# Performance work log

Measured on AMD Instinct MI355X. Metric: run time of the kernel, lower is better.

The kernel has to match this reference:

```python
import jax, jax.numpy as jnp
import numpy as np

EPS = 1e-7  # keras backend epsilon

def setup_inputs() -> dict:
    key = jax.random.key(0)
    k1, k2, k3, k4, k5 = jax.random.split(key, 5)
    B, S, D, A = 64, 2048, 512, 256
    x = jax.random.normal(k1, (B, S, D), dtype=jnp.float32)
    mask = jax.random.randint(k2, (B, S), 0, 2) > 0
    # keras 'normal' initializer: RandomNormal(stddev=0.05)
    W = 0.05 * jax.random.normal(k3, (D, A), dtype=jnp.float32)
    b = 0.05 * jax.random.normal(k4, (A,), dtype=jnp.float32)
    u = 0.05 * jax.random.normal(k5, (A, 1), dtype=jnp.float32)
    return {"x": x, "mask": mask, "W": W, "b": b, "u": u}

def reference(x, mask, W, b, u):
    # x: [B,S,D], W: [D,A], b: [A], u: [A,1]
    uit = jnp.tanh(jnp.einsum('bsd,da->bsa', x, W) + b)   # [B,S,A]
    ait = jnp.einsum('bsa,a->bs', uit, u[:, 0])           # [B,S]
    ait = jnp.exp(ait)
    ait = ait * mask.astype(x.dtype)
    ait = ait / (jnp.sum(ait, axis=1, keepdims=True) + EPS)  # [B,S]
    return jnp.einsum('bsd,bs->bd', x, ait)               # [B,D]
```

## Files before the change

kernel.cpp:

```cpp
#include <hip/hip_runtime.h>
#include <stdint.h>

#define B_ 64
#define S_ 2048
#define D_ 512
#define A_ 256
#define TM 32
#define TPB 16
#define NBLK 256
#define EPS 1e-7f

typedef short bf16x8 __attribute__((ext_vector_type(8)));
typedef float f32x4  __attribute__((ext_vector_type(4)));

#define WS_WT   0
#define WS_PART 262144
#define WS_ZP   786432
#define WS_FLAG 787456

__device__ __forceinline__ uint32_t f32pair_to_bf16(float a, float b) {
  uint32_t ua = __float_as_uint(a), ub = __float_as_uint(b);
  ua = (ua + 0x7fffu + ((ua >> 16) & 1u)) >> 16;
  ub = (ub + 0x7fffu + ((ub >> 16) & 1u)) & 0xffff0000u;
  return ua | ub;
}

__global__ __launch_bounds__(256) void prep_kernel(
    const float* __restrict__ W, const void* __restrict__ mask,
    uint16_t* __restrict__ Wt, int* __restrict__ flag)
{
  int i = blockIdx.x * 256 + threadIdx.x;
  if (i < A_ * D_) {
    int a = i >> 9;
    int d = i & (D_ - 1);
    uint32_t u = __float_as_uint(W[d * A_ + a]);
    u = (u + 0x7fffu + ((u >> 16) & 1u)) >> 16;
    Wt[i] = (uint16_t)u;
  }
  if (blockIdx.x == 0 && threadIdx.x < 64) {
    const uint32_t* mw = (const uint32_t*)mask;
    int hit = 0;
    for (int k = 0; k < 16; ++k) {
      uint32_t v = mw[threadIdx.x + 64 * k];
      uint32_t b0 = v & 0xff, b1 = (v >> 8) & 0xff, b2 = (v >> 16) & 0xff, b3 = v >> 24;
      if (b0 <= 1u && b1 <= 1u && b2 <= 1u && b3 <= 1u && (b1 | b2 | b3)) hit = 1;
    }
    hit = __any(hit);
    if (threadIdx.x == 0) *flag = hit ? 1 : 0;
  }
}

__global__ __launch_bounds__(512, 2) void att_main(
    const float* __restrict__ x, const void* __restrict__ mask,
    const float* __restrict__ bias, const float* __restrict__ uvec,
    const uint16_t* __restrict__ Wt, float* __restrict__ part,
    float* __restrict__ Zpart, const int* __restrict__ flag)
{
  __shared__ uint16_t xs[2][TM * D_];
  __shared__ float sp[8][TM];
  __shared__ float ev[TM];

  const int tid = threadIdx.x;
  const int l  = tid & 63, w  = tid >> 6;
  const int lr = l & 15,   lg = l >> 4;
  const int bx = blockIdx.x;
  const int b  = bx >> 2;
  const int s0 = (bx & 3) * (TM * TPB);
  const float* xb = x + ((size_t)b * S_ + s0) * D_;
  const int mflag = *flag;

  bf16x8 bfr[32];
  {
    const uint16_t* wtb = Wt + (size_t)(w * 32 + lr) * D_;
    #pragma unroll
    for (int ks = 0; ks < 16; ++ks)
      #pragma unroll
      for (int nt = 0; nt < 2; ++nt)
        bfr[ks * 2 + nt] = *(const bf16x8*)(wtb + nt * 16 * D_ + ks * 32 + lg * 8);
  }
  float bn[2], un[2];
  #pragma unroll
  for (int nt = 0; nt < 2; ++nt) {
    int n = w * 32 + nt * 16 + lr;
    bn[nt] = bias[n];
    un[nt] = uvec[n];
  }

  float num_acc = 0.0f;
  float zacc    = 0.0f;

  float4 v[4][2];
  #pragma unroll
  for (int c = 0; c < 4; ++c) {
    int q = c * 512 + tid;
    const float* src = xb + (q >> 6) * D_ + (q & 63) * 8;
    v[c][0] = *(const float4*)src;
    v[c][1] = *(const float4*)(src + 4);
  }

  for (int t = 0; t < TPB; ++t) {
    uint16_t* buf = xs[t & 1];

    #pragma unroll
    for (int c = 0; c < 4; ++c) {
      int q = c * 512 + tid;
      int row = q >> 6, cb = q & 63;
      uint4 pk;
      pk.x = f32pair_to_bf16(v[c][0].x, v[c][0].y);
      pk.y = f32pair_to_bf16(v[c][0].z, v[c][0].w);
      pk.z = f32pair_to_bf16(v[c][1].x, v[c][1].y);
      pk.w = f32pair_to_bf16(v[c][1].z, v[c][1].w);
      *(uint4*)(&buf[row * D_ + (cb ^ (row & 7)) * 8]) = pk;
    }
    __syncthreads();

    if (t + 1 < TPB) {
      const float* xt = xb + (size_t)(t + 1) * TM * D_;
      #pragma unroll
      for (int c = 0; c < 4; ++c) {
        int q = c * 512 + tid;
        const float* src = xt + (q >> 6) * D_ + (q & 63) * 8;
        v[c][0] = *(const float4*)src;
        v[c][1] = *(const float4*)(src + 4);
      }
    }

    f32x4 acc[2][2];
    #pragma unroll
    for (int mt = 0; mt < 2; ++mt)
      #pragma unroll
      for (int nt = 0; nt < 2; ++nt)
        acc[mt][nt] = (f32x4){0.f, 0.f, 0.f, 0.f};

    #pragma unroll
    for (int ks = 0; ks < 16; ++ks) {
      bf16x8 af[2];
      #pragma unroll
      for (int mt = 0; mt < 2; ++mt)
        af[mt] = *(const bf16x8*)(&buf[(mt * 16 + lr) * D_ + (((ks * 4 + lg) ^ (lr & 7)) * 8)]);
      #pragma unroll
      for (int mt = 0; mt < 2; ++mt)
        #pragma unroll
        for (int nt = 0; nt < 2; ++nt)
          acc[mt][nt] = __builtin_amdgcn_mfma_f32_16x16x32_bf16(af[mt], bfr[ks * 2 + nt], acc[mt][nt], 0, 0, 0);
    }

    #pragma unroll
    for (int mt = 0; mt < 2; ++mt) {
      #pragma unroll
      for (int r = 0; r < 4; ++r) {
        float ssum = 0.0f;
        #pragma unroll
        for (int nt = 0; nt < 2; ++nt) {
          float vv = acc[mt][nt][r] + bn[nt];
          float av = fabsf(vv);
          float e2 = __expf(-2.0f * av);
          float th = 1.0f - 2.0f * e2 * __builtin_amdgcn_rcpf(1.0f + e2);
          ssum += copysignf(th, vv) * un[nt];
        }
        ssum += __shfl_xor(ssum, 1);
        ssum += __shfl_xor(ssum, 2);
        ssum += __shfl_xor(ssum, 4);
        ssum += __shfl_xor(ssum, 8);
        if (lr == 0) sp[w][mt * 16 + lg * 4 + r] = ssum;
      }
    }
    __syncthreads();

    if (tid < TM) {
      float score = 0.0f;
      #pragma unroll
      for (int ww = 0; ww < 8; ++ww) score += sp[ww][tid];
      int midx = b * S_ + s0 + t * TM + tid;
      int mv = mflag ? (((const unsigned char*)mask)[midx] != 0)
                     : (((const int*)mask)[midx] != 0);
      float e = mv ? __expf(score) : 0.0f;
      ev[tid] = e;
      float tot = e;
      #pragma unroll
      for (int o = 1; o < TM; o <<= 1) tot += __shfl_xor(tot, o);
      if (tid == 0) zacc += tot;
    }
    __syncthreads();

    {
      int c = tid >> 3, wo = (tid & 7) >> 1;
      #pragma unroll 8
      for (int s = 0; s < TM; ++s) {
        uint32_t vv = *(const uint32_t*)(&buf[s * D_ + (c ^ (s & 7)) * 8 + wo * 2]);
        float xv = (tid & 1) ? __uint_as_float(vv & 0xffff0000u)
                             : __uint_as_float(vv << 16);
        num_acc = fmaf(ev[s], xv, num_acc);
      }
    }
  }

  part[(size_t)bx * D_ + tid] = num_acc;
  if (tid == 0) Zpart[bx] = zacc;
}

__global__ __launch_bounds__(256) void scale_kernel(
    const float* __restrict__ part, const float* __restrict__ Zpart,
    float* __restrict__ out)
{
  int idx = blockIdx.x * 256 + threadIdx.x;
  int b = idx >> 9;
  int d = idx & (D_ - 1);
  float s = 0.0f, z = 0.0f;
  #pragma unroll
  for (int g = 0; g < 4; ++g) {
    s += part[(size_t)(b * 4 + g) * D_ + d];
    z += Zpart[b * 4 + g];
  }
  out[idx] = s / (z + EPS);
}

extern "C" void kernel_launch(void* const* d_in, const int* in_sizes, int n_in,
                              void* d_out, int out_size, void* d_ws, size_t ws_size,
                              hipStream_t stream)
{
  const float* x    = (const float*)d_in[0];
  const void*  mask = d_in[1];
  const float* W    = (const float*)d_in[2];
  const float* bias = (const float*)d_in[3];
  const float* u    = (const float*)d_in[4];
  float* out = (float*)d_out;

  char* ws = (char*)d_ws;
  uint16_t* Wt  = (uint16_t*)(ws + WS_WT);
  float* part   = (float*)(ws + WS_PART);
  float* Zpart  = (float*)(ws + WS_ZP);
  int*   flag   = (int*)(ws + WS_FLAG);

  prep_kernel<<<(A_ * D_ + 255) / 256, 256, 0, stream>>>(W, mask, Wt, flag);
  att_main<<<NBLK, 512, 0, stream>>>(x, mask, bias, u, Wt, part, Zpart, flag);
  scale_kernel<<<(B_ * D_ + 255) / 256, 256, 0, stream>>>(part, Zpart, out);
}
```

Before: 379.0 us.

## Stream x tiles via direct global-to-LDS loads and cut per-tile barriers

Replaces the register-staged prefetch of x with global_load_lds DMA into an fp32 LDS staging buffer, loaded two tiles ahead and converted to bf16 one tile ahead inside the loop. The mask is preloaded once per block, every wave computes the scores redundantly and broadcasts them with readlane, and one barrier per tile is dropped. The 16-lane reductions use DPP instead of shuffles. This aims to free registers and overlap memory traffic with MFMA work, at the cost of 64KB more LDS, which may lower occupancy below the two blocks per CU requested.

```diff
diff --git a/kernel.cpp b/kernel.cpp
--- a/kernel.cpp
+++ b/kernel.cpp
@@ -25,6 +25,24 @@
   return ua | ub;
 }
 
+__device__ __forceinline__ void gload_lds16(const float* g, float* l) {
+  __builtin_amdgcn_global_load_lds(
+      (const __attribute__((address_space(1))) uint32_t*)g,
+      (__attribute__((address_space(3))) uint32_t*)l, 16, 0, 0);
+}
+
+__device__ __forceinline__ float row16_sum(float x) {
+  int v = __float_as_int(x);
+  x += __int_as_float(__builtin_amdgcn_update_dpp(v, v, 0xB1, 0xF, 0xF, false));
+  v = __float_as_int(x);
+  x += __int_as_float(__builtin_amdgcn_update_dpp(v, v, 0x4E, 0xF, 0xF, false));
+  v = __float_as_int(x);
+  x += __int_as_float(__builtin_amdgcn_update_dpp(v, v, 0x141, 0xF, 0xF, false));
+  v = __float_as_int(x);
+  x += __int_as_float(__builtin_amdgcn_update_dpp(v, v, 0x128, 0xF, 0xF, false));
+  return x;
+}
+
 __global__ __launch_bounds__(256) void prep_kernel(
     const float* __restrict__ W, const void* __restrict__ mask,
     uint16_t* __restrict__ Wt, int* __restrict__ flag)
@@ -56,9 +74,10 @@
     const uint16_t* __restrict__ Wt, float* __restrict__ part,
     float* __restrict__ Zpart, const int* __restrict__ flag)
 {
+  __shared__ float xf[TM * D_];
   __shared__ uint16_t xs[2][TM * D_];
   __shared__ float sp[8][TM];
-  __shared__ float ev[TM];
+  __shared__ float me[TM * TPB];
 
   const int tid = threadIdx.x;
   const int l  = tid & 63, w  = tid >> 6;
@@ -69,6 +88,13 @@
   const float* xb = x + ((size_t)b * S_ + s0) * D_;
   const int mflag = *flag;
 
+  {
+    int midx = b * S_ + s0 + tid;
+    int mv = mflag ? (((const unsigned char*)mask)[midx] != 0)
+                   : (((const int*)mask)[midx] != 0);
+    me[tid] = mv ? 1.0f : 0.0f;
+  }
+
   bf16x8 bfr[32];
   {
     const uint16_t* wtb = Wt + (size_t)(w * 32 + lr) * D_;
@@ -89,41 +115,39 @@
   float num_acc = 0.0f;
   float zacc    = 0.0f;
 
-  float4 v[4][2];
+  #pragma unroll
+  for (int i = 0; i < 8; ++i) {
+    int id = w * 8 + i, row = id >> 1, h = id & 1;
+    gload_lds16(xb + row * D_ + (2 * l + h) * 4, &xf[row * D_ + h * 256]);
+  }
+  __syncthreads();
+
   #pragma unroll
   for (int c = 0; c < 4; ++c) {
-    int q = c * 512 + tid;
-    const float* src = xb + (q >> 6) * D_ + (q & 63) * 8;
-    v[c][0] = *(const float4*)src;
-    v[c][1] = *(const float4*)(src + 4);
-  }
-
+    int row = c * 8 + w;
+    float4 lo = *(const float4*)&xf[row * D_ + l * 4];
+    float4 hi = *(const float4*)&xf[row * D_ + 256 + l * 4];
+    uint4 pk;
+    pk.x = f32pair_to_bf16(lo.x, lo.y);
+    pk.y = f32pair_to_bf16(lo.z, lo.w);
+    pk.z = f32pair_to_bf16(hi.x, hi.y);
+    pk.w = f32pair_to_bf16(hi.z, hi.w);
+    *(uint4*)(&xs[0][row * D_ + ((l ^ (row & 7)) * 8)]) = pk;
+  }
+  __syncthreads();
+
+  {
+    const float* xt = xb + (size_t)TM * D_;
+    #pragma unroll
+    for (int i = 0; i < 8; ++i) {
+      int id = w * 8 + i, row = id >> 1, h = id & 1;
+      gload_lds16(xt + row * D_ + (2 * l + h) * 4, &xf[row * D_ + h * 256]);
+    }
+  }
+
+  #pragma unroll 2
   for (int t = 0; t < TPB; ++t) {
-    uint16_t* buf = xs[t & 1];
-
-    #pragma unroll
-    for (int c = 0; c < 4; ++c) {
-      int q = c * 512 + tid;
-      int row = q >> 6, cb = q & 63;
-      uint4 pk;
-      pk.x = f32pair_to_bf16(v[c][0].x, v[c][0].y);
-      pk.y = f32pair_to_bf16(v[c][0].z, v[c][0].w);
-      pk.z = f32pair_to_bf16(v[c][1].x, v[c][1].y);
-      pk.w = f32pair_to_bf16(v[c][1].z, v[c][1].w);
-      *(uint4*)(&buf[row * D_ + (cb ^ (row & 7)) * 8]) = pk;
-    }
-    __syncthreads();
-
-    if (t + 1 < TPB) {
-      const float* xt = xb + (size_t)(t + 1) * TM * D_;
-      #pragma unroll
-      for (int c = 0; c < 4; ++c) {
-        int q = c * 512 + tid;
-        const float* src = xt + (q >> 6) * D_ + (q & 63) * 8;
-        v[c][0] = *(const float4*)src;
-        v[c][1] = *(const float4*)(src + 4);
-      }
-    }
+    const uint16_t* buf = xs[t & 1];
 
     f32x4 acc[2][2];
     #pragma unroll
@@ -158,39 +182,64 @@
           float th = 1.0f - 2.0f * e2 * __builtin_amdgcn_rcpf(1.0f + e2);
           ssum += copysignf(th, vv) * un[nt];
         }
-        ssum += __shfl_xor(ssum, 1);
-        ssum += __shfl_xor(ssum, 2);
-        ssum += __shfl_xor(ssum, 4);
-        ssum += __shfl_xor(ssum, 8);
+        ssum = row16_sum(ssum);
         if (lr == 0) sp[w][mt * 16 + lg * 4 + r] = ssum;
       }
     }
     __syncthreads();
 
-    if (tid < TM) {
-      float score = 0.0f;
-      #pragma unroll
-      for (int ww = 0; ww < 8; ++ww) score += sp[ww][tid];
-      int midx = b * S_ + s0 + t * TM + tid;
-      int mv = mflag ? (((const unsigned char*)mask)[midx] != 0)
-                     : (((const int*)mask)[midx] != 0);
-      float e = mv ? __expf(score) : 0.0f;
-      ev[tid] = e;
-      float tot = e;
-      #pragma unroll
-      for (int o = 1; o < TM; o <<= 1) tot += __shfl_xor(tot, o);
-      if (tid == 0) zacc += tot;
-    }
-    __syncthreads();
+    if (t + 1 < TPB) {
+      uint16_t* nb = xs[(t + 1) & 1];
+      #pragma unroll
+      for (int c = 0; c < 4; ++c) {
+        int row = c * 8 + w;
+        float4 lo = *(const float4*)&xf[row * D_ + l * 4];
+        float4 hi = *(const float4*)&xf[row * D_ + 256 + l * 4];
+        uint4 pk;
+        pk.x = f32pair_to_bf16(lo.x, lo.y);
+        pk.y = f32pair_to_bf16(lo.z, lo.w);
+        pk.z = f32pair_to_bf16(hi.x, hi.y);
+        pk.w = f32pair_to_bf16(hi.z, hi.w);
+        *(uint4*)(&nb[row * D_ + ((l ^ (row & 7)) * 8)]) = pk;
+      }
+    }
+
+    float eval = 0.0f;
+    if (l < 32) {
+      float sc = 0.0f;
+      #pragma unroll
+      for (int ww = 0; ww < 8; ++ww) sc += sp[ww][l];
+      eval = me[t * TM + l] * __expf(sc);
+    }
+    if (w == 0 && l < 32) {
+      float tot = eval;
+      tot += __shfl_xor(tot, 1);
+      tot += __shfl_xor(tot, 2);
+      tot += __shfl_xor(tot, 4);
+      tot += __shfl_xor(tot, 8);
+      tot += __shfl_xor(tot, 16);
+      if (l == 0) zacc += tot;
+    }
 
     {
-      int c = tid >> 3, wo = (tid & 7) >> 1;
-      #pragma unroll 8
+      int cw = tid >> 3, wo = (tid & 7) >> 1;
+      #pragma unroll
       for (int s = 0; s < TM; ++s) {
-        uint32_t vv = *(const uint32_t*)(&buf[s * D_ + (c ^ (s & 7)) * 8 + wo * 2]);
+        float e = __int_as_float(__builtin_amdgcn_readlane(__float_as_int(eval), s));
+        uint32_t vv = *(const uint32_t*)(&buf[s * D_ + (cw ^ (s & 7)) * 8 + wo * 2]);
         float xv = (tid & 1) ? __uint_as_float(vv & 0xffff0000u)
                              : __uint_as_float(vv << 16);
-        num_acc = fmaf(ev[s], xv, num_acc);
+        num_acc = fmaf(e, xv, num_acc);
+      }
+    }
+    __syncthreads();
+
+    if (t + 2 < TPB) {
+      const float* xt = xb + (size_t)(t + 2) * TM * D_;
+      #pragma unroll
+      for (int i = 0; i < 8; ++i) {
+        int id = w * 8 + i, row = id >> 1, h = id & 1;
+        gload_lds16(xt + row * D_ + (2 * l + h) * 4, &xf[row * D_ + h * 256]);
       }
     }
   }
```

Measured after the change: 372.0 us. No clear change (-1.9%).
